# Kernel optimization log

Hardware: AMD Instinct MI355X
Metric: run time of the kernel (lower is better)

Reference implementation:

```python
import jax, jax.numpy as jnp
import numpy as np

B, Cin, Cout = 2, 32, 16
D, H, W = 48, 64, 128
K = 3
EPS = 1e-5  # BatchNorm3d default eps


def setup_inputs() -> dict:
    key = jax.random.key(0)
    ks = jax.random.split(key, 6)
    return {
        "x": jax.random.normal(ks[0], (B, Cin, D, H, W), jnp.float32),
        "weight": jax.random.normal(ks[1], (Cout, Cin, K, K, K), jnp.float32) * 0.05,
        "gamma": jax.random.uniform(ks[2], (Cout,), jnp.float32, minval=0.5, maxval=1.5),
        "beta": jax.random.normal(ks[3], (Cout,), jnp.float32) * 0.1,
        "running_mean": jax.random.normal(ks[4], (Cout,), jnp.float32) * 0.1,
        "running_var": jax.random.uniform(ks[5], (Cout,), jnp.float32, minval=0.5, maxval=1.5),
    }


def _binarize(v):
    # forward: sign(v) in {-1, 0, +1}; backward (STE): hardtanh grad (pass-through on |v|<=1)
    clipped = jnp.clip(v, -1.0, 1.0)
    return clipped + jax.lax.stop_gradient(jnp.sign(v) - clipped)


def reference(x, weight, gamma, beta, running_mean, running_var):
    b, c, d, h, w = x.shape
    # trilinear upsample, scale (1,2,2), align_corners=False (half-pixel centers)
    x = jax.image.resize(x, (b, c, d, 2 * h, 2 * w), method="trilinear")
    # binarize activations and weights; XNOR-style per-output-channel scale alpha = mean|W|
    xb = _binarize(x)
    alpha = jnp.mean(jnp.abs(weight), axis=(1, 2, 3, 4), keepdims=True)  # [Cout,1,1,1,1]
    wb = _binarize(weight) * alpha
    y = jax.lax.conv_general_dilated(
        xb, wb,
        window_strides=(1, 1, 1),
        padding=[(1, 1), (1, 1), (1, 1)],
        dimension_numbers=("NCDHW", "OIDHW", "NCDHW"),
    )  # [B, Cout, D, 2H, 2W]
    # fused BatchNorm3d (inference form) + ReLU
    inv = gamma / jnp.sqrt(running_var + EPS)
    shift = beta - running_mean * inv
    y = y * inv[None, :, None, None, None] + shift[None, :, None, None, None]
    return jax.nn.relu(y)
```

## Files before the change

### kernel.cpp

```cpp
#include <hip/hip_runtime.h>
#include <hip/hip_bf16.h>
#include <stdint.h>

#define BB   2
#define CIN  32
#define COUT 16
#define DD   48
#define HIN  64
#define WIN  128
#define H2   128
#define W2   256
#define PLANE_WORDS (H2 * W2)

__global__ __launch_bounds__(512) void ibc3d_prep(
    const float* __restrict__ wgt, const float* __restrict__ gamma,
    const float* __restrict__ beta, const float* __restrict__ rmean,
    const float* __restrict__ rvar, uint32_t* __restrict__ bw,
    float* __restrict__ scale, float* __restrict__ shift)
{
    int t = threadIdx.x;
    if (t < 27 * 16) {
        int tap = t >> 4, co = t & 15;
        uint32_t word = 0;
        for (int ci = 0; ci < CIN; ++ci) {
            float v = wgt[(co * CIN + ci) * 27 + tap];
            word |= (v > 0.0f ? 1u : 0u) << ci;
        }
        bw[t] = word;
    } else if (t < 27 * 16 + 16) {
        int co = t - 27 * 16;
        double s = 0.0;
        for (int i = 0; i < CIN * 27; ++i)
            s += fabs((double)wgt[co * CIN * 27 + i]);
        float alpha = (float)(s / (double)(CIN * 27));
        float inv = gamma[co] / sqrtf(rvar[co] + 1e-5f);
        scale[co] = alpha * inv;
        shift[co] = beta[co] - rmean[co] * inv;
    }
}

__device__ __forceinline__ uint32_t pack_word(const float* __restrict__ x,
                                              int b, int d, int h2, int w2)
{
    int m = h2 >> 1, dh = h2 & 1;
    int n = w2 >> 1, dwp = w2 & 1;
    int rA = m + dh - 1;
    int rB = rA + 1;
    double wA = dh ? 0.75 : 0.25;
    double wB = 1.0 - wA;
    rA = rA < 0 ? 0 : rA;
    rB = rB > (HIN - 1) ? (HIN - 1) : rB;
    int cA = n + dwp - 1;
    int cB = cA + 1;
    double wC = dwp ? 0.75 : 0.25;
    double wD = 1.0 - wC;
    cA = cA < 0 ? 0 : cA;
    cB = cB > (WIN - 1) ? (WIN - 1) : cB;

    const float* xp = x + ((size_t)b * CIN * DD + d) * (HIN * WIN);
    int oA = rA * WIN, oB = rB * WIN;
    uint32_t word = 0;
    for (int ci = 0; ci < CIN; ++ci) {
        const float* xc = xp + (size_t)ci * (DD * HIN * WIN);
        float a0 = xc[oA + cA], a1 = xc[oA + cB];
        float b0 = xc[oB + cA], b1 = xc[oB + cB];
        double t0 = wA * (double)a0 + wB * (double)b0;
        double t1 = wA * (double)a1 + wB * (double)b1;
        double v  = wC * t0 + wD * t1;
        word |= (v >= 0.0 ? 1u : 0u) << ci;
    }
    return word;
}

__global__ __launch_bounds__(256) void ibc3d_pack2(
    const float* __restrict__ x, uint32_t* __restrict__ bx,
    int b_start, int nplanes)
{
    int idx = blockIdx.x * 256 + threadIdx.x;
    if (idx >= nplanes * PLANE_WORDS) return;
    int w2 = idx & (W2 - 1);
    int h2 = (idx >> 8) & (H2 - 1);
    int rl = idx >> 15;
    int d  = rl % DD;
    int b  = b_start + rl / DD;
    bx[idx] = pack_word(x, b, d, h2, w2);
}

__global__ __launch_bounds__(256) void ibc3d_conv2(
    const uint32_t* __restrict__ bx, const uint32_t* __restrict__ bwg,
    const float* __restrict__ scaleg, const float* __restrict__ shiftg,
    float* __restrict__ out, int b_start)
{
    __shared__ uint32_t sbw[27 * 16];
    __shared__ float sscale[16];
    __shared__ float sshift[16];
    int tid = threadIdx.x;
    for (int i = tid; i < 27 * 16; i += 256) sbw[i] = bwg[i];
    if (tid < 16) { sscale[tid] = scaleg[tid]; sshift[tid] = shiftg[tid]; }
    __syncthreads();

    int bid   = blockIdx.x;
    int h2    = bid & (H2 - 1);
    int plane = bid >> 7;
    int d     = plane % DD;
    int b     = b_start + plane / DD;
    int w2    = tid;

    int acc[16];
#pragma unroll
    for (int c = 0; c < 16; ++c) acc[c] = 0;
    int nv = 0;

    for (int kd = 0; kd < 3; ++kd) {
        int dd = d + kd - 1;
        if (dd < 0 || dd >= DD) continue;
        const uint32_t* bxp = bx + (size_t)(plane + kd - 1) * PLANE_WORDS;
        for (int kh = 0; kh < 3; ++kh) {
            int hh = h2 + kh - 1;
            if (hh < 0 || hh >= H2) continue;
            for (int kw = 0; kw < 3; ++kw) {
                int ww = w2 + kw - 1;
                if (ww < 0 || ww >= W2) continue;
                uint32_t word = bxp[hh * W2 + ww];
                nv += 1;
                int tap = kd * 9 + kh * 3 + kw;
#pragma unroll
                for (int co = 0; co < 16; ++co)
                    acc[co] += __popc(word ^ sbw[tap * 16 + co]);
            }
        }
    }

    float base = 32.0f * (float)nv;
#pragma unroll
    for (int co = 0; co < 16; ++co) {
        float y = (base - 2.0f * (float)acc[co]) * sscale[co] + sshift[co];
        y = y > 0.0f ? y : 0.0f;
        size_t oidx = (((size_t)(b * COUT + co) * DD + d) * H2 + h2) * W2 + w2;
        out[oidx] = y;
    }
}

__global__ __launch_bounds__(256) void ibc3d_fused(
    const float* __restrict__ x, const float* __restrict__ wgt,
    const float* __restrict__ gamma, const float* __restrict__ beta,
    const float* __restrict__ rmean, const float* __restrict__ rvar,
    float* __restrict__ out)
{
    __shared__ uint32_t sbw[27 * 16];
    __shared__ float sscale[16];
    __shared__ float sshift[16];
    __shared__ uint32_t sw[3][10][264];

    int tid = threadIdx.x;
    for (int t = tid; t < 27 * 16; t += 256) {
        int tap = t >> 4, co = t & 15;
        uint32_t word = 0;
        for (int ci = 0; ci < CIN; ++ci) {
            float v = wgt[(co * CIN + ci) * 27 + tap];
            word |= (v > 0.0f ? 1u : 0u) << ci;
        }
        sbw[t] = word;
    }
    if (tid < 16) {
        int co = tid;
        double s = 0.0;
        for (int i = 0; i < CIN * 27; ++i)
            s += fabs((double)wgt[co * CIN * 27 + i]);
        float alpha = (float)(s / (double)(CIN * 27));
        float inv = gamma[co] / sqrtf(rvar[co] + 1e-5f);
        sscale[co] = alpha * inv;
        sshift[co] = beta[co] - rmean[co] * inv;
    }

    int bid = blockIdx.x;
    int hq  = bid & 15;
    int r   = bid >> 4;
    int b   = r / DD;
    int d   = r % DD;
    int h2base = hq * 8;

    for (int i = tid; i < 3 * 10 * 258; i += 256) {
        int kd  = i / 2580;
        int rem = i - kd * 2580;
        int ri  = rem / 258;
        int ciw = rem - ri * 258;
        int dd = d + kd - 1;
        int h2 = h2base - 1 + ri;
        int w2 = ciw - 1;
        uint32_t word = 0;
        if (dd >= 0 && dd < DD && h2 >= 0 && h2 < H2 && w2 >= 0 && w2 < W2)
            word = pack_word(x, b, dd, h2, w2);
        sw[kd][ri][ciw] = word;
    }
    __syncthreads();

    int w2 = tid;
    for (int p = 0; p < 8; ++p) {
        int h2 = h2base + p;
        int acc[16];
#pragma unroll
        for (int c = 0; c < 16; ++c) acc[c] = 0;
        int nv = 0;
        for (int kd = 0; kd < 3; ++kd) {
            int dd = d + kd - 1;
            if (dd < 0 || dd >= DD) continue;
            for (int kh = 0; kh < 3; ++kh) {
                int hh = h2 + kh - 1;
                if (hh < 0 || hh >= H2) continue;
                for (int kw = 0; kw < 3; ++kw) {
                    int ww = w2 + kw - 1;
                    if (ww < 0 || ww >= W2) continue;
                    uint32_t word = sw[kd][p + kh][w2 + kw];
                    nv += 1;
                    int tap = kd * 9 + kh * 3 + kw;
#pragma unroll
                    for (int co = 0; co < 16; ++co)
                        acc[co] += __popc(word ^ sbw[tap * 16 + co]);
                }
            }
        }
        float base = 32.0f * (float)nv;
#pragma unroll
        for (int co = 0; co < 16; ++co) {
            float y = (base - 2.0f * (float)acc[co]) * sscale[co] + sshift[co];
            y = y > 0.0f ? y : 0.0f;
            size_t oidx = (((size_t)(b * COUT + co) * DD + d) * H2 + h2) * W2 + w2;
            out[oidx] = y;
        }
    }
}

extern "C" void kernel_launch(void* const* d_in, const int* in_sizes, int n_in,
                              void* d_out, int out_size, void* d_ws, size_t ws_size,
                              hipStream_t stream)
{
    (void)in_sizes; (void)n_in; (void)out_size;
    const float* x     = (const float*)d_in[0];
    const float* wgt   = (const float*)d_in[1];
    const float* gamma = (const float*)d_in[2];
    const float* beta  = (const float*)d_in[3];
    const float* rmean = (const float*)d_in[4];
    const float* rvar  = (const float*)d_in[5];
    float* out = (float*)d_out;

    const size_t HDR = 4096;
    const size_t bx_full = (size_t)BB * DD * PLANE_WORDS * 4;
    const size_t bx_half = (size_t)DD * PLANE_WORDS * 4;

    if (d_ws != nullptr && ws_size >= HDR + bx_full) {
        uint8_t* ws = (uint8_t*)d_ws;
        uint32_t* bw    = (uint32_t*)ws;
        float*    scale = (float*)(ws + 2048);
        float*    shift = (float*)(ws + 2112);
        uint32_t* bx    = (uint32_t*)(ws + HDR);
        ibc3d_prep<<<1, 512, 0, stream>>>(wgt, gamma, beta, rmean, rvar, bw, scale, shift);
        int nplanes = BB * DD;
        ibc3d_pack2<<<nplanes * (PLANE_WORDS / 256), 256, 0, stream>>>(x, bx, 0, nplanes);
        ibc3d_conv2<<<nplanes * H2, 256, 0, stream>>>(bx, bw, scale, shift, out, 0);
    } else if (d_ws != nullptr && ws_size >= HDR + bx_half) {
        uint8_t* ws = (uint8_t*)d_ws;
        uint32_t* bw    = (uint32_t*)ws;
        float*    scale = (float*)(ws + 2048);
        float*    shift = (float*)(ws + 2112);
        uint32_t* bx    = (uint32_t*)(ws + HDR);
        ibc3d_prep<<<1, 512, 0, stream>>>(wgt, gamma, beta, rmean, rvar, bw, scale, shift);
        for (int b = 0; b < BB; ++b) {
            ibc3d_pack2<<<DD * (PLANE_WORDS / 256), 256, 0, stream>>>(x, bx, b, DD);
            ibc3d_conv2<<<DD * H2, 256, 0, stream>>>(bx, bw, scale, shift, out, b);
        }
    } else {
        ibc3d_fused<<<BB * DD * (H2 / 8), 256, 0, stream>>>(
            x, wgt, gamma, beta, rmean, rvar, out);
    }
}
```

Measured before the change: 173.6 us.

## Pack four upsampled outputs per thread with float math and double fallback

The pack kernel now has each thread own one input pixel and produce the 2x2 block of upsampled binarized words from a shared 3x3 neighbourhood. This replaces per-output 4-tap gathers and double-precision interpolation with fp32 fixed weights, and falls back to double only when a value is near zero so the sign still matches. The conv kernel drops its shared-memory staging and barrier, reading weights and scale directly through uniform global loads. It also fully unrolls the tap loops and computes the valid-tap count in closed form. The trade-off is more register pressure and a divergent fallback branch in the pack kernel.

```diff
diff --git a/kernel.cpp b/kernel.cpp
--- a/kernel.cpp
+++ b/kernel.cpp
@@ -72,72 +72,123 @@
     return word;
 }
 
-__global__ __launch_bounds__(256) void ibc3d_pack2(
+__global__ __launch_bounds__(256) void ibc3d_packq(
     const float* __restrict__ x, uint32_t* __restrict__ bx,
     int b_start, int nplanes)
 {
     int idx = blockIdx.x * 256 + threadIdx.x;
-    if (idx >= nplanes * PLANE_WORDS) return;
-    int w2 = idx & (W2 - 1);
-    int h2 = (idx >> 8) & (H2 - 1);
-    int rl = idx >> 15;
-    int d  = rl % DD;
-    int b  = b_start + rl / DD;
-    bx[idx] = pack_word(x, b, d, h2, w2);
-}
-
-__global__ __launch_bounds__(256) void ibc3d_conv2(
+    int n  = idx & (WIN - 1);
+    int m  = (idx >> 7) & (HIN - 1);
+    int pl = idx >> 13;
+    if (pl >= nplanes) return;
+    int d  = pl % DD;
+    int b  = b_start + pl / DD;
+
+    int rm1 = m > 0 ? m - 1 : 0;
+    int rp1 = m < HIN - 1 ? m + 1 : HIN - 1;
+    int cm1 = n > 0 ? n - 1 : 0;
+    int cp1 = n < WIN - 1 ? n + 1 : WIN - 1;
+
+    const float* xp = x + ((size_t)b * CIN * DD + d) * (HIN * WIN);
+    int o0 = rm1 * WIN, o1 = m * WIN, o2 = rp1 * WIN;
+
+    uint32_t w00 = 0, w01 = 0, w10 = 0, w11 = 0;
+#pragma unroll 4
+    for (int ci = 0; ci < CIN; ++ci) {
+        const float* xc = xp + (size_t)ci * (DD * HIN * WIN);
+        float a00 = xc[o0 + cm1], a01 = xc[o0 + n], a02 = xc[o0 + cp1];
+        float a10 = xc[o1 + cm1], a11 = xc[o1 + n], a12 = xc[o1 + cp1];
+        float a20 = xc[o2 + cm1], a21 = xc[o2 + n], a22 = xc[o2 + cp1];
+
+        float u0r0 = 0.25f * a00 + 0.75f * a01, u1r0 = 0.75f * a01 + 0.25f * a02;
+        float u0r1 = 0.25f * a10 + 0.75f * a11, u1r1 = 0.75f * a11 + 0.25f * a12;
+        float u0r2 = 0.25f * a20 + 0.75f * a21, u1r2 = 0.75f * a21 + 0.25f * a22;
+
+        float v00 = 0.25f * u0r0 + 0.75f * u0r1;
+        float v01 = 0.25f * u1r0 + 0.75f * u1r1;
+        float v10 = 0.75f * u0r1 + 0.25f * u0r2;
+        float v11 = 0.75f * u1r1 + 0.25f * u1r2;
+
+        uint32_t s00, s01, s10, s11;
+        float amin = fminf(fminf(fabsf(v00), fabsf(v01)),
+                           fminf(fabsf(v10), fabsf(v11)));
+        if (__builtin_expect(amin < 1e-5f, 0)) {
+            double d00 = a00, d01 = a01, d02 = a02;
+            double d10 = a10, d11 = a11, d12 = a12;
+            double d20 = a20, d21 = a21, d22 = a22;
+            double e0r0 = 0.25 * d00 + 0.75 * d01, e1r0 = 0.75 * d01 + 0.25 * d02;
+            double e0r1 = 0.25 * d10 + 0.75 * d11, e1r1 = 0.75 * d11 + 0.25 * d12;
+            double e0r2 = 0.25 * d20 + 0.75 * d21, e1r2 = 0.75 * d21 + 0.25 * d22;
+            s00 = (0.25 * e0r0 + 0.75 * e0r1) >= 0.0;
+            s01 = (0.25 * e1r0 + 0.75 * e1r1) >= 0.0;
+            s10 = (0.75 * e0r1 + 0.25 * e0r2) >= 0.0;
+            s11 = (0.75 * e1r1 + 0.25 * e1r2) >= 0.0;
+        } else {
+            s00 = v00 >= 0.0f;
+            s01 = v01 >= 0.0f;
+            s10 = v10 >= 0.0f;
+            s11 = v11 >= 0.0f;
+        }
+        w00 |= s00 << ci; w01 |= s01 << ci;
+        w10 |= s10 << ci; w11 |= s11 << ci;
+    }
+
+    size_t base = (size_t)pl * PLANE_WORDS + (size_t)(2 * m) * W2 + 2 * n;
+    *(uint2*)(bx + base)      = make_uint2(w00, w01);
+    *(uint2*)(bx + base + W2) = make_uint2(w10, w11);
+}
+
+__global__ __launch_bounds__(256) void ibc3d_conv3(
     const uint32_t* __restrict__ bx, const uint32_t* __restrict__ bwg,
     const float* __restrict__ scaleg, const float* __restrict__ shiftg,
     float* __restrict__ out, int b_start)
 {
-    __shared__ uint32_t sbw[27 * 16];
-    __shared__ float sscale[16];
-    __shared__ float sshift[16];
-    int tid = threadIdx.x;
-    for (int i = tid; i < 27 * 16; i += 256) sbw[i] = bwg[i];
-    if (tid < 16) { sscale[tid] = scaleg[tid]; sshift[tid] = shiftg[tid]; }
-    __syncthreads();
-
     int bid   = blockIdx.x;
     int h2    = bid & (H2 - 1);
     int plane = bid >> 7;
     int d     = plane % DD;
     int b     = b_start + plane / DD;
-    int w2    = tid;
+    int w2    = threadIdx.x;
 
     int acc[16];
 #pragma unroll
     for (int c = 0; c < 16; ++c) acc[c] = 0;
-    int nv = 0;
-
+
+#pragma unroll
     for (int kd = 0; kd < 3; ++kd) {
         int dd = d + kd - 1;
         if (dd < 0 || dd >= DD) continue;
         const uint32_t* bxp = bx + (size_t)(plane + kd - 1) * PLANE_WORDS;
+#pragma unroll
         for (int kh = 0; kh < 3; ++kh) {
             int hh = h2 + kh - 1;
             if (hh < 0 || hh >= H2) continue;
+            const uint32_t* brow = bxp + hh * W2;
+#pragma unroll
             for (int kw = 0; kw < 3; ++kw) {
                 int ww = w2 + kw - 1;
-                if (ww < 0 || ww >= W2) continue;
-                uint32_t word = bxp[hh * W2 + ww];
-                nv += 1;
-                int tap = kd * 9 + kh * 3 + kw;
-#pragma unroll
-                for (int co = 0; co < 16; ++co)
-                    acc[co] += __popc(word ^ sbw[tap * 16 + co]);
+                if (ww >= 0 && ww < W2) {
+                    uint32_t word = brow[ww];
+                    int tap = kd * 9 + kh * 3 + kw;
+#pragma unroll
+                    for (int co = 0; co < 16; ++co)
+                        acc[co] += __popc(word ^ bwg[tap * 16 + co]);
+                }
             }
         }
     }
 
-    float base = 32.0f * (float)nv;
+    int nd = 1 + (d > 0)  + (d < DD - 1);
+    int nh = 1 + (h2 > 0) + (h2 < H2 - 1);
+    int nw = 1 + (w2 > 0) + (w2 < W2 - 1);
+    float base = 32.0f * (float)(nd * nh * nw);
+
+    size_t obase = (((size_t)(b * COUT) * DD + d) * H2 + h2) * W2 + w2;
 #pragma unroll
     for (int co = 0; co < 16; ++co) {
-        float y = (base - 2.0f * (float)acc[co]) * sscale[co] + sshift[co];
+        float y = (base - 2.0f * (float)acc[co]) * scaleg[co] + shiftg[co];
         y = y > 0.0f ? y : 0.0f;
-        size_t oidx = (((size_t)(b * COUT + co) * DD + d) * H2 + h2) * W2 + w2;
-        out[oidx] = y;
+        out[obase + (size_t)co * (DD * H2 * W2)] = y;
     }
 }
 
@@ -256,8 +307,8 @@
         uint32_t* bx    = (uint32_t*)(ws + HDR);
         ibc3d_prep<<<1, 512, 0, stream>>>(wgt, gamma, beta, rmean, rvar, bw, scale, shift);
         int nplanes = BB * DD;
-        ibc3d_pack2<<<nplanes * (PLANE_WORDS / 256), 256, 0, stream>>>(x, bx, 0, nplanes);
-        ibc3d_conv2<<<nplanes * H2, 256, 0, stream>>>(bx, bw, scale, shift, out, 0);
+        ibc3d_packq<<<nplanes * 32, 256, 0, stream>>>(x, bx, 0, nplanes);
+        ibc3d_conv3<<<nplanes * H2, 256, 0, stream>>>(bx, bw, scale, shift, out, 0);
     } else if (d_ws != nullptr && ws_size >= HDR + bx_half) {
         uint8_t* ws = (uint8_t*)d_ws;
         uint32_t* bw    = (uint32_t*)ws;
@@ -266,8 +317,8 @@
         uint32_t* bx    = (uint32_t*)(ws + HDR);
         ibc3d_prep<<<1, 512, 0, stream>>>(wgt, gamma, beta, rmean, rvar, bw, scale, shift);
         for (int b = 0; b < BB; ++b) {
-            ibc3d_pack2<<<DD * (PLANE_WORDS / 256), 256, 0, stream>>>(x, bx, b, DD);
-            ibc3d_conv2<<<DD * H2, 256, 0, stream>>>(bx, bw, scale, shift, out, b);
+            ibc3d_packq<<<DD * 32, 256, 0, stream>>>(x, bx, b, DD);
+            ibc3d_conv3<<<DD * H2, 256, 0, stream>>>(bx, bw, scale, shift, out, b);
         }
     } else {
         ibc3d_fused<<<BB * DD * (H2 / 8), 256, 0, stream>>>(
```

New measurement: 162.1 us. 1.07x faster.
